# Kernel tuning notes

Hardware: AMD Instinct MI355X
Metric: run time of the kernel (lower is better)

## Reference

```python
import jax, jax.numpy as jnp
import numpy as np

M = 768   # num edges
N = 768   # num loops (== M because original tiles image_x with len(edge_x) for both)
C = 256
IMG = 1024
CAT = 3 * C + IMG  # 1792, 'sharing' suffix without '1d'/'noimage'
EPS = 1e-4


def _lin_block(x, W, b):
    # LinearBlock: Linear + ReLU
    return jax.nn.relu(x @ W + b)


def _pred_head(x, W1, b1, W2, b2):
    # Sequential(LinearBlock(256,64), Linear(64,1)) -> sigmoid -> flatten
    return jax.nn.sigmoid(_lin_block(x, W1, b1) @ W2 + b2).reshape(-1)


def setup_inputs() -> dict:
    key = jax.random.key(0)
    ks = jax.random.split(key, 24)
    s = 0.02
    return {
        "edge_x": jax.random.normal(ks[0], (M, C), jnp.float32),
        "loop_x": jax.random.normal(ks[1], (N, C), jnp.float32),
        "image_x": jax.random.normal(ks[2], (1, IMG), jnp.float32),
        "loop_edge_masks": (jax.random.uniform(ks[3], (N, M)) < 0.3).astype(jnp.float32),
        "edge_conflict_mask": (jax.random.uniform(ks[4], (M, M)) < 0.1).astype(jnp.float32),
        "loop_conflict_mask": (jax.random.uniform(ks[5], (N, N)) < 0.1).astype(jnp.float32),
        "loop_masks": jax.random.uniform(ks[6], (N, 64), jnp.float32),      # pass-through only
        "loop_edge_indices": jax.random.randint(ks[7], (N,), 0, M, jnp.int32),  # unused ('1d' off)
        "edge_info": jax.random.normal(ks[8], (M, 4), jnp.float32),         # unused ('1d' off)
        "W_e3": jax.random.normal(ks[9], (CAT, C), jnp.float32) * s,
        "b_e3": jnp.zeros((C,), jnp.float32),
        "W_l3": jax.random.normal(ks[10], (CAT, C), jnp.float32) * s,
        "b_l3": jnp.zeros((C,), jnp.float32),
        "W_ep1": jax.random.normal(ks[11], (C, 64), jnp.float32) * s,
        "b_ep1": jnp.zeros((64,), jnp.float32),
        "W_ep2": jax.random.normal(ks[12], (64, 1), jnp.float32) * s,
        "b_ep2": jnp.zeros((1,), jnp.float32),
        "W_lp1": jax.random.normal(ks[13], (C, 64), jnp.float32) * s,
        "b_lp1": jnp.zeros((64,), jnp.float32),
        "W_lp2": jax.random.normal(ks[14], (64, 1), jnp.float32) * s,
        "b_lp2": jnp.zeros((1,), jnp.float32),
    }


def reference(edge_x, loop_x, image_x, loop_edge_masks, edge_conflict_mask,
              loop_conflict_mask, loop_masks, loop_edge_indices, edge_info,
              W_e3, b_e3, W_l3, b_l3, W_ep1, b_ep1, W_ep2, b_ep2,
              W_lp1, b_lp1, W_lp2, b_lp2):
    # iteration-0 predictions (appended to results in original)
    e0 = _pred_head(edge_x, W_ep1, b_ep1, W_ep2, b_ep2)  # [M]
    l0 = _pred_head(loop_x, W_lp1, b_lp1, W_lp2, b_lp2)  # [N]

    # weights[n, m] = mask * |loop_pred[n] - edge_pred[m]|
    w = loop_edge_masks * jnp.abs(l0[:, None] - e0[None, :])  # [N, M]

    # weighted broadcast sums (einsum == unsqueeze-multiply-sum in the original)
    edge_x_from_loop = jnp.einsum('nm,nc->mc', w, loop_x) \
        / jnp.maximum(w.sum(0), EPS)[:, None]               # [M, C]
    loop_x_from_edge = jnp.einsum('nm,mc->nc', w, edge_x) \
        / jnp.maximum(w.sum(1), EPS)[:, None]               # [N, C]

    # conflict-masked max pooling (materializes [M,M,C]/[N,N,C] like the original)
    edge_x_from_conflict = jnp.max(edge_conflict_mask[:, :, None] * edge_x[None, :, :], axis=1)
    loop_x_from_conflict = jnp.max(loop_conflict_mask[:, :, None] * loop_x[None, :, :], axis=1)

    img_e = jnp.broadcast_to(image_x, (edge_x.shape[0], image_x.shape[1]))
    img_l = jnp.broadcast_to(image_x, (loop_x.shape[0], image_x.shape[1]))

    edge_x2 = _lin_block(jnp.concatenate([edge_x, edge_x_from_loop, edge_x_from_conflict, img_e], axis=-1), W_e3, b_e3)
    loop_x2 = _lin_block(jnp.concatenate([loop_x, loop_x_from_edge, loop_x_from_conflict, img_l], axis=-1), W_l3, b_l3)

    e1 = _pred_head(edge_x2, W_ep1, b_ep1, W_ep2, b_ep2)
    l1 = _pred_head(loop_x2, W_lp1, b_lp1, W_lp2, b_lp2)

    # original returns results=[[e0,l0,masks,loop_masks],[e1,l1,masks,loop_masks]];
    # masks are constant pass-throughs, so we return the predictions concatenated.
    return jnp.concatenate([e0, l0, e1, l1])  # [2*(M+N)] = [3072]
```

## Files before the change

kernel.cpp:

```cpp
#include <hip/hip_runtime.h>
#include <hip/hip_bf16.h>
#include <math.h>

#define MM 768
#define CC 256
#define EPSV 1e-4f

__device__ __forceinline__ float sigmoidf_(float x) { return 1.0f / (1.0f + expf(-x)); }

__global__ __launch_bounds__(256) void k_prep(
    const float* __restrict__ edge_x, const float* __restrict__ loop_x,
    const float* __restrict__ image_x,
    const float* __restrict__ ecm, const float* __restrict__ lcm,
    const float* __restrict__ We3, const float* __restrict__ Wl3,
    const float* __restrict__ Wep1, const float* __restrict__ bep1,
    const float* __restrict__ Wep2, const float* __restrict__ bep2,
    const float* __restrict__ Wlp1, const float* __restrict__ blp1,
    const float* __restrict__ Wlp2, const float* __restrict__ blp2,
    float* __restrict__ out, float* __restrict__ efc, float* __restrict__ lfc,
    float* __restrict__ imgpart)
{
    int bid = blockIdx.x;
    int t   = threadIdx.x;

    if (bid < 1536) {
        __shared__ int   s_cnt;
        __shared__ int   s_idx[MM];
        __shared__ float s_val[MM];
        bool isLoop = bid >= MM;
        int  m      = bid & (MM - 1);
        const float* mask = isLoop ? lcm : ecm;
        const float* x    = isLoop ? loop_x : edge_x;
        float*       o    = isLoop ? lfc : efc;

        if (t == 0) s_cnt = 0;
        __syncthreads();
        int lane = t & 63;
        #pragma unroll
        for (int r = 0; r < 3; ++r) {
            int j = t + r * 256;
            float v = mask[m * MM + j];
            bool nz = (v != 0.0f);
            unsigned long long b = __ballot(nz);
            int prefix = __popcll(b & ((1ull << lane) - 1ull));
            int cntw   = __popcll(b);
            int base = 0;
            if (lane == 0 && cntw) base = atomicAdd(&s_cnt, cntw);
            base = __shfl(base, 0, 64);
            if (nz) { s_idx[base + prefix] = j; s_val[base + prefix] = v; }
        }
        __syncthreads();
        int cnt = s_cnt;
        float init = (cnt < MM) ? 0.0f : -INFINITY;
        float a0 = init, a1 = init, a2 = init, a3 = init;
        int i = 0;
        for (; i + 4 <= cnt; i += 4) {
            a0 = fmaxf(a0, s_val[i + 0] * x[s_idx[i + 0] * CC + t]);
            a1 = fmaxf(a1, s_val[i + 1] * x[s_idx[i + 1] * CC + t]);
            a2 = fmaxf(a2, s_val[i + 2] * x[s_idx[i + 2] * CC + t]);
            a3 = fmaxf(a3, s_val[i + 3] * x[s_idx[i + 3] * CC + t]);
        }
        for (; i < cnt; ++i)
            a0 = fmaxf(a0, s_val[i] * x[s_idx[i] * CC + t]);
        o[m * CC + t] = fmaxf(fmaxf(a0, a1), fmaxf(a2, a3));

    } else if (bid < 1920) {
        int wave = t >> 6, lane = t & 63;
        int row  = (bid - 1536) * 4 + wave;
        const float *x, *W1, *b1, *W2;
        float b2v;
        if (row < MM) { x = edge_x + row * CC;        W1 = Wep1; b1 = bep1; W2 = Wep2; b2v = bep2[0]; }
        else          { x = loop_x + (row - MM) * CC; W1 = Wlp1; b1 = blp1; W2 = Wlp2; b2v = blp2[0]; }

        float a0 = 0.f, a1 = 0.f, a2 = 0.f, a3 = 0.f;
        for (int cc = 0; cc < CC; cc += 4) {
            float4 xv = *reinterpret_cast<const float4*>(x + cc);
            a0 = fmaf(xv.x, W1[(cc + 0) * 64 + lane], a0);
            a1 = fmaf(xv.y, W1[(cc + 1) * 64 + lane], a1);
            a2 = fmaf(xv.z, W1[(cc + 2) * 64 + lane], a2);
            a3 = fmaf(xv.w, W1[(cc + 3) * 64 + lane], a3);
        }
        float h = fmaxf(b1[lane] + ((a0 + a1) + (a2 + a3)), 0.0f);
        float p = h * W2[lane];
        #pragma unroll
        for (int off = 32; off; off >>= 1) p += __shfl_xor(p, off, 64);
        if (lane == 0) out[row] = sigmoidf_(p + b2v);

    } else {
        int sub   = bid - 1920;
        int chunk = sub & 3;
        int head  = sub >> 2;
        const float* W = head ? Wl3 : We3;
        int k0 = chunk * 256;
        float s = 0.0f;
        #pragma unroll 4
        for (int k = 0; k < 256; ++k)
            s = fmaf(image_x[k0 + k], W[(768 + k0 + k) * CC + t], s);
        imgpart[head * 1024 + chunk * 256 + t] = s;
    }
}

__global__ __launch_bounds__(512) void k_bsum(
    const float* __restrict__ lem, const float* __restrict__ edge_x,
    const float* __restrict__ loop_x, const float* __restrict__ pred,
    float* __restrict__ efl_p0, float* __restrict__ efl_p1,
    float* __restrict__ lfe_p0, float* __restrict__ lfe_p1)
{
    __shared__ float4 s_wv4[MM];
    __shared__ float  s_pw[8 * 4];
    __shared__ float  s_sum[4];
    __shared__ float  s_red[4 * 16 * 64];
    float* s_wv = reinterpret_cast<float*>(s_wv4);

    int bid  = blockIdx.x;
    int t    = threadIdx.x;
    int pair = bid >> 1, sh = bid & 1;
    const float* e0 = pred;
    const float* l0 = pred + MM;

    bool isE = pair < 192;
    int  r0  = (isE ? pair : pair - 192) * 4;
    const float* ownp = isE ? e0 : l0;
    const float* othp = isE ? l0 : e0;

    float own0 = ownp[r0], own1 = ownp[r0 + 1], own2 = ownp[r0 + 2], own3 = ownp[r0 + 3];

    int i_ = t & 3;
    float myown = own0;
    if (i_ == 1) myown = own1; else if (i_ == 2) myown = own2; else if (i_ == 3) myown = own3;
    float psum = 0.f;
    #pragma unroll
    for (int k = 0; k < 6; ++k) {
        int idx = t + k * 512;
        int s = idx >> 2;
        float lm = isE ? lem[s * MM + r0 + i_] : lem[(r0 + i_) * MM + s];
        float wv = lm * fabsf(othp[s] - myown);
        s_wv[idx] = wv;
        psum += wv;
    }
    #pragma unroll
    for (int off = 4; off < 64; off <<= 1) psum += __shfl_xor(psum, off, 64);
    int wave = t >> 6, lane = t & 63;
    if (lane < 4) s_pw[wave * 4 + lane] = psum;
    __syncthreads();
    if (t < 4) {
        float s = 0.f;
        #pragma unroll
        for (int w = 0; w < 8; ++w) s += s_pw[w * 4 + t];
        s_sum[t] = fmaxf(s, EPSV);
    }

    const float* xsrc = isE ? loop_x : edge_x;
    int s_base = sh * 384 + wave * 48;
    float acc[4][4];
    #pragma unroll
    for (int i = 0; i < 4; ++i)
        #pragma unroll
        for (int c = 0; c < 4; ++c) acc[i][c] = 0.f;

    #pragma unroll 4
    for (int j = 0; j < 48; ++j) {
        int s = s_base + j;
        float4 w4 = s_wv4[s];
        float4 xv = *reinterpret_cast<const float4*>(xsrc + s * CC + lane * 4);
        acc[0][0] = fmaf(w4.x, xv.x, acc[0][0]); acc[0][1] = fmaf(w4.x, xv.y, acc[0][1]);
        acc[0][2] = fmaf(w4.x, xv.z, acc[0][2]); acc[0][3] = fmaf(w4.x, xv.w, acc[0][3]);
        acc[1][0] = fmaf(w4.y, xv.x, acc[1][0]); acc[1][1] = fmaf(w4.y, xv.y, acc[1][1]);
        acc[1][2] = fmaf(w4.y, xv.z, acc[1][2]); acc[1][3] = fmaf(w4.y, xv.w, acc[1][3]);
        acc[2][0] = fmaf(w4.z, xv.x, acc[2][0]); acc[2][1] = fmaf(w4.z, xv.y, acc[2][1]);
        acc[2][2] = fmaf(w4.z, xv.z, acc[2][2]); acc[2][3] = fmaf(w4.z, xv.w, acc[2][3]);
        acc[3][0] = fmaf(w4.w, xv.x, acc[3][0]); acc[3][1] = fmaf(w4.w, xv.y, acc[3][1]);
        acc[3][2] = fmaf(w4.w, xv.z, acc[3][2]); acc[3][3] = fmaf(w4.w, xv.w, acc[3][3]);
    }

    if (wave >= 4) {
        #pragma unroll
        for (int i = 0; i < 4; ++i)
            #pragma unroll
            for (int c = 0; c < 4; ++c)
                s_red[(wave - 4) * 1024 + (i * 4 + c) * 64 + lane] = acc[i][c];
    }
    __syncthreads();
    if (wave < 4) {
        #pragma unroll
        for (int i = 0; i < 4; ++i)
            #pragma unroll
            for (int c = 0; c < 4; ++c)
                acc[i][c] += s_red[wave * 1024 + (i * 4 + c) * 64 + lane];
    }
    __syncthreads();
    if (wave == 2 || wave == 3) {
        #pragma unroll
        for (int i = 0; i < 4; ++i)
            #pragma unroll
            for (int c = 0; c < 4; ++c)
                s_red[(wave - 2) * 1024 + (i * 4 + c) * 64 + lane] = acc[i][c];
    }
    __syncthreads();
    if (wave < 2) {
        #pragma unroll
        for (int i = 0; i < 4; ++i)
            #pragma unroll
            for (int c = 0; c < 4; ++c)
                acc[i][c] += s_red[wave * 1024 + (i * 4 + c) * 64 + lane];
    }
    __syncthreads();
    if (wave == 1) {
        #pragma unroll
        for (int i = 0; i < 4; ++i)
            #pragma unroll
            for (int c = 0; c < 4; ++c)
                s_red[(i * 4 + c) * 64 + lane] = acc[i][c];
    }
    __syncthreads();
    if (wave == 0) {
        float* outp = isE ? (sh ? efl_p1 : efl_p0) : (sh ? lfe_p1 : lfe_p0);
        #pragma unroll
        for (int i = 0; i < 4; ++i) {
            float inv = 1.0f / s_sum[i];
            float4 o;
            o.x = (acc[i][0] + s_red[(i * 4 + 0) * 64 + lane]) * inv;
            o.y = (acc[i][1] + s_red[(i * 4 + 1) * 64 + lane]) * inv;
            o.z = (acc[i][2] + s_red[(i * 4 + 2) * 64 + lane]) * inv;
            o.w = (acc[i][3] + s_red[(i * 4 + 3) * 64 + lane]) * inv;
            *reinterpret_cast<float4*>(outp + (r0 + i) * CC + lane * 4) = o;
        }
    }
}

__global__ __launch_bounds__(512) void k_cat(
    const float* __restrict__ edge_x, const float* __restrict__ loop_x,
    const float* __restrict__ efl_p0, const float* __restrict__ efl_p1,
    const float* __restrict__ lfe_p0, const float* __restrict__ lfe_p1,
    const float* __restrict__ efc, const float* __restrict__ lfc,
    const float* __restrict__ We3, const float* __restrict__ be3,
    const float* __restrict__ Wl3, const float* __restrict__ bl3,
    const float* __restrict__ imgpart,
    const float* __restrict__ Wep1, const float* __restrict__ bep1,
    const float* __restrict__ Wep2, const float* __restrict__ bep2,
    const float* __restrict__ Wlp1, const float* __restrict__ blp1,
    const float* __restrict__ Wlp2, const float* __restrict__ blp2,
    float* __restrict__ out)
{
    __shared__ float s_red[4 * 16 * 64];
    __shared__ float s_act[4 * CC];
    __shared__ float s_h[8 * 64];

    int head = blockIdx.y;
    const float* W   = head ? Wl3 : We3;
    const float* b   = head ? bl3 : be3;
    const float* x0  = head ? loop_x : edge_x;
    const float* x1a = head ? lfe_p0 : efl_p0;
    const float* x1b = head ? lfe_p1 : efl_p1;
    const float* x2  = head ? lfc : efc;
    const float* ip  = imgpart + head * 1024;

    int m0 = blockIdx.x * 4;
    int t  = threadIdx.x;
    int wave = t >> 6, lane = t & 63;

    float acc[4][4];
    #pragma unroll
    for (int i = 0; i < 4; ++i)
        #pragma unroll
        for (int c = 0; c < 4; ++c) acc[i][c] = 0.f;

    int k0 = wave * 96;
    for (int jj = 0; jj < 96; jj += 4) {
        int k = k0 + jj;
        float4 xr[4];
        if (k < 256) {
            #pragma unroll
            for (int i = 0; i < 4; ++i)
                xr[i] = *reinterpret_cast<const float4*>(x0 + (m0 + i) * CC + k);
        } else if (k < 512) {
            int kk = k - 256;
            #pragma unroll
            for (int i = 0; i < 4; ++i) {
                float4 a = *reinterpret_cast<const float4*>(x1a + (m0 + i) * CC + kk);
                float4 bb = *reinterpret_cast<const float4*>(x1b + (m0 + i) * CC + kk);
                xr[i].x = a.x + bb.x; xr[i].y = a.y + bb.y;
                xr[i].z = a.z + bb.z; xr[i].w = a.w + bb.w;
            }
        } else {
            int kk = k - 512;
            #pragma unroll
            for (int i = 0; i < 4; ++i)
                xr[i] = *reinterpret_cast<const float4*>(x2 + (m0 + i) * CC + kk);
        }
        #pragma unroll
        for (int j = 0; j < 4; ++j) {
            float4 wv = *reinterpret_cast<const float4*>(W + (k + j) * CC + lane * 4);
            float xj0 = reinterpret_cast<const float*>(&xr[0])[j];
            float xj1 = reinterpret_cast<const float*>(&xr[1])[j];
            float xj2 = reinterpret_cast<const float*>(&xr[2])[j];
            float xj3 = reinterpret_cast<const float*>(&xr[3])[j];
            acc[0][0] = fmaf(xj0, wv.x, acc[0][0]); acc[0][1] = fmaf(xj0, wv.y, acc[0][1]);
            acc[0][2] = fmaf(xj0, wv.z, acc[0][2]); acc[0][3] = fmaf(xj0, wv.w, acc[0][3]);
            acc[1][0] = fmaf(xj1, wv.x, acc[1][0]); acc[1][1] = fmaf(xj1, wv.y, acc[1][1]);
            acc[1][2] = fmaf(xj1, wv.z, acc[1][2]); acc[1][3] = fmaf(xj1, wv.w, acc[1][3]);
            acc[2][0] = fmaf(xj2, wv.x, acc[2][0]); acc[2][1] = fmaf(xj2, wv.y, acc[2][1]);
            acc[2][2] = fmaf(xj2, wv.z, acc[2][2]); acc[2][3] = fmaf(xj2, wv.w, acc[2][3]);
            acc[3][0] = fmaf(xj3, wv.x, acc[3][0]); acc[3][1] = fmaf(xj3, wv.y, acc[3][1]);
            acc[3][2] = fmaf(xj3, wv.z, acc[3][2]); acc[3][3] = fmaf(xj3, wv.w, acc[3][3]);
        }
    }

    if (wave >= 4) {
        #pragma unroll
        for (int i = 0; i < 4; ++i)
            #pragma unroll
            for (int c = 0; c < 4; ++c)
                s_red[(wave - 4) * 1024 + (i * 4 + c) * 64 + lane] = acc[i][c];
    }
    __syncthreads();
    if (wave < 4) {
        #pragma unroll
        for (int i = 0; i < 4; ++i)
            #pragma unroll
            for (int c = 0; c < 4; ++c)
                acc[i][c] += s_red[wave * 1024 + (i * 4 + c) * 64 + lane];
    }
    __syncthreads();
    if (wave == 2 || wave == 3) {
        #pragma unroll
        for (int i = 0; i < 4; ++i)
            #pragma unroll
            for (int c = 0; c < 4; ++c)
                s_red[(wave - 2) * 1024 + (i * 4 + c) * 64 + lane] = acc[i][c];
    }
    __syncthreads();
    if (wave < 2) {
        #pragma unroll
        for (int i = 0; i < 4; ++i)
            #pragma unroll
            for (int c = 0; c < 4; ++c)
                acc[i][c] += s_red[wave * 1024 + (i * 4 + c) * 64 + lane];
    }
    __syncthreads();
    if (wave == 1) {
        #pragma unroll
        for (int i = 0; i < 4; ++i)
            #pragma unroll
            for (int c = 0; c < 4; ++c)
                s_red[(i * 4 + c) * 64 + lane] = acc[i][c];
    }
    __syncthreads();
    if (wave == 0) {
        float4 b4  = *reinterpret_cast<const float4*>(b + lane * 4);
        float4 i0  = *reinterpret_cast<const float4*>(ip + lane * 4);
        float4 i1  = *reinterpret_cast<const float4*>(ip + 256 + lane * 4);
        float4 i2  = *reinterpret_cast<const float4*>(ip + 512 + lane * 4);
        float4 i3  = *reinterpret_cast<const float4*>(ip + 768 + lane * 4);
        float bias[4] = { b4.x + i0.x + i1.x + i2.x + i3.x,
                          b4.y + i0.y + i1.y + i2.y + i3.y,
                          b4.z + i0.z + i1.z + i2.z + i3.z,
                          b4.w + i0.w + i1.w + i2.w + i3.w };
        #pragma unroll
        for (int i = 0; i < 4; ++i) {
            float4 o;
            o.x = fmaxf(acc[i][0] + s_red[(i * 4 + 0) * 64 + lane] + bias[0], 0.f);
            o.y = fmaxf(acc[i][1] + s_red[(i * 4 + 1) * 64 + lane] + bias[1], 0.f);
            o.z = fmaxf(acc[i][2] + s_red[(i * 4 + 2) * 64 + lane] + bias[2], 0.f);
            o.w = fmaxf(acc[i][3] + s_red[(i * 4 + 3) * 64 + lane] + bias[3], 0.f);
            *reinterpret_cast<float4*>(s_act + i * CC + lane * 4) = o;
        }
    }
    __syncthreads();

    int row = wave >> 1, khalf = wave & 1;
    const float* W1 = head ? Wlp1 : Wep1;
    const float* b1 = head ? blp1 : bep1;
    const float* W2 = head ? Wlp2 : Wep2;
    float b2v       = head ? blp2[0] : bep2[0];
    const float* xr = s_act + row * CC + khalf * 128;

    float a0 = 0.f, a1 = 0.f, a2 = 0.f, a3 = 0.f;
    for (int cc = 0; cc < 128; cc += 4) {
        float4 xv = *reinterpret_cast<const float4*>(xr + cc);
        int kb = khalf * 128 + cc;
        a0 = fmaf(xv.x, W1[(kb + 0) * 64 + lane], a0);
        a1 = fmaf(xv.y, W1[(kb + 1) * 64 + lane], a1);
        a2 = fmaf(xv.z, W1[(kb + 2) * 64 + lane], a2);
        a3 = fmaf(xv.w, W1[(kb + 3) * 64 + lane], a3);
    }
    s_h[wave * 64 + lane] = (a0 + a1) + (a2 + a3);
    __syncthreads();
    if (khalf == 0) {
        float hv = fmaxf(b1[lane] + s_h[wave * 64 + lane] + s_h[(wave + 1) * 64 + lane], 0.0f);
        float p = hv * W2[lane];
        #pragma unroll
        for (int off = 32; off; off >>= 1) p += __shfl_xor(p, off, 64);
        if (lane == 0) out[1536 + head * MM + m0 + row] = sigmoidf_(p + b2v);
    }
}

extern "C" void kernel_launch(void* const* d_in, const int* in_sizes, int n_in,
                              void* d_out, int out_size, void* d_ws, size_t ws_size,
                              hipStream_t stream)
{
    const float* edge_x  = (const float*)d_in[0];
    const float* loop_x  = (const float*)d_in[1];
    const float* image_x = (const float*)d_in[2];
    const float* lem     = (const float*)d_in[3];
    const float* ecm     = (const float*)d_in[4];
    const float* lcm     = (const float*)d_in[5];
    const float* We3  = (const float*)d_in[9];
    const float* be3  = (const float*)d_in[10];
    const float* Wl3  = (const float*)d_in[11];
    const float* bl3  = (const float*)d_in[12];
    const float* Wep1 = (const float*)d_in[13];
    const float* bep1 = (const float*)d_in[14];
    const float* Wep2 = (const float*)d_in[15];
    const float* bep2 = (const float*)d_in[16];
    const float* Wlp1 = (const float*)d_in[17];
    const float* blp1 = (const float*)d_in[18];
    const float* Wlp2 = (const float*)d_in[19];
    const float* blp2 = (const float*)d_in[20];

    float* out = (float*)d_out;
    float* ws  = (float*)d_ws;

    float* imgpart = ws;
    float* efl_p0  = ws + 2048;
    float* efl_p1  = efl_p0 + MM * CC;
    float* lfe_p0  = efl_p1 + MM * CC;
    float* lfe_p1  = lfe_p0 + MM * CC;
    float* efc     = lfe_p1 + MM * CC;
    float* lfc     = efc + MM * CC;

    k_prep<<<1928, 256, 0, stream>>>(edge_x, loop_x, image_x, ecm, lcm,
                                     We3, Wl3,
                                     Wep1, bep1, Wep2, bep2,
                                     Wlp1, blp1, Wlp2, blp2,
                                     out, efc, lfc, imgpart);

    k_bsum<<<768, 512, 0, stream>>>(lem, edge_x, loop_x, out,
                                    efl_p0, efl_p1, lfe_p0, lfe_p1);

    k_cat<<<dim3(192, 2), 512, 0, stream>>>(edge_x, loop_x,
                                            efl_p0, efl_p1, lfe_p0, lfe_p1,
                                            efc, lfc,
                                            We3, be3, Wl3, bl3, imgpart,
                                            Wep1, bep1, Wep2, bep2,
                                            Wlp1, blp1, Wlp2, blp2, out);
}
```

Baseline: 170.1 us.

## Move conflict max-pool into middle kernel and drop split-K partial buffers

The conflict-masked max pooling moves out of the first kernel into the second, which now has 384 weighted-sum blocks followed by 768 blocks that each handle two max-pool rows, sharing memory through a union. The weighted-sum blocks now cover all 768 source rows instead of splitting them across two blocks, so only one partial buffer per side is written and the concat GEMM no longer adds two partials. The goal is to shrink the first kernel so it finishes sooner, balance work across launches, and cut intermediate memory traffic. In exchange each weighted-sum block runs a loop twice as long, and there are half as many of them.

```diff
diff --git a/kernel.cpp b/kernel.cpp
--- a/kernel.cpp
+++ b/kernel.cpp
@@ -11,62 +11,19 @@
 __global__ __launch_bounds__(256) void k_prep(
     const float* __restrict__ edge_x, const float* __restrict__ loop_x,
     const float* __restrict__ image_x,
-    const float* __restrict__ ecm, const float* __restrict__ lcm,
     const float* __restrict__ We3, const float* __restrict__ Wl3,
     const float* __restrict__ Wep1, const float* __restrict__ bep1,
     const float* __restrict__ Wep2, const float* __restrict__ bep2,
     const float* __restrict__ Wlp1, const float* __restrict__ blp1,
     const float* __restrict__ Wlp2, const float* __restrict__ blp2,
-    float* __restrict__ out, float* __restrict__ efc, float* __restrict__ lfc,
-    float* __restrict__ imgpart)
+    float* __restrict__ out, float* __restrict__ imgpart)
 {
     int bid = blockIdx.x;
     int t   = threadIdx.x;
 
-    if (bid < 1536) {
-        __shared__ int   s_cnt;
-        __shared__ int   s_idx[MM];
-        __shared__ float s_val[MM];
-        bool isLoop = bid >= MM;
-        int  m      = bid & (MM - 1);
-        const float* mask = isLoop ? lcm : ecm;
-        const float* x    = isLoop ? loop_x : edge_x;
-        float*       o    = isLoop ? lfc : efc;
-
-        if (t == 0) s_cnt = 0;
-        __syncthreads();
-        int lane = t & 63;
-        #pragma unroll
-        for (int r = 0; r < 3; ++r) {
-            int j = t + r * 256;
-            float v = mask[m * MM + j];
-            bool nz = (v != 0.0f);
-            unsigned long long b = __ballot(nz);
-            int prefix = __popcll(b & ((1ull << lane) - 1ull));
-            int cntw   = __popcll(b);
-            int base = 0;
-            if (lane == 0 && cntw) base = atomicAdd(&s_cnt, cntw);
-            base = __shfl(base, 0, 64);
-            if (nz) { s_idx[base + prefix] = j; s_val[base + prefix] = v; }
-        }
-        __syncthreads();
-        int cnt = s_cnt;
-        float init = (cnt < MM) ? 0.0f : -INFINITY;
-        float a0 = init, a1 = init, a2 = init, a3 = init;
-        int i = 0;
-        for (; i + 4 <= cnt; i += 4) {
-            a0 = fmaxf(a0, s_val[i + 0] * x[s_idx[i + 0] * CC + t]);
-            a1 = fmaxf(a1, s_val[i + 1] * x[s_idx[i + 1] * CC + t]);
-            a2 = fmaxf(a2, s_val[i + 2] * x[s_idx[i + 2] * CC + t]);
-            a3 = fmaxf(a3, s_val[i + 3] * x[s_idx[i + 3] * CC + t]);
-        }
-        for (; i < cnt; ++i)
-            a0 = fmaxf(a0, s_val[i] * x[s_idx[i] * CC + t]);
-        o[m * CC + t] = fmaxf(fmaxf(a0, a1), fmaxf(a2, a3));
-
-    } else if (bid < 1920) {
+    if (bid < 384) {
         int wave = t >> 6, lane = t & 63;
-        int row  = (bid - 1536) * 4 + wave;
+        int row  = bid * 4 + wave;
         const float *x, *W1, *b1, *W2;
         float b2v;
         if (row < MM) { x = edge_x + row * CC;        W1 = Wep1; b1 = bep1; W2 = Wep2; b2v = bep2[0]; }
@@ -87,7 +44,7 @@
         if (lane == 0) out[row] = sigmoidf_(p + b2v);
 
     } else {
-        int sub   = bid - 1920;
+        int sub   = bid - 384;
         int chunk = sub & 3;
         int head  = sub >> 2;
         const float* W = head ? Wl3 : We3;
@@ -100,138 +57,181 @@
     }
 }
 
-__global__ __launch_bounds__(512) void k_bsum(
+__global__ __launch_bounds__(512) void k_mid(
     const float* __restrict__ lem, const float* __restrict__ edge_x,
     const float* __restrict__ loop_x, const float* __restrict__ pred,
-    float* __restrict__ efl_p0, float* __restrict__ efl_p1,
-    float* __restrict__ lfe_p0, float* __restrict__ lfe_p1)
+    const float* __restrict__ ecm, const float* __restrict__ lcm,
+    float* __restrict__ efl, float* __restrict__ lfe,
+    float* __restrict__ efc, float* __restrict__ lfc)
 {
-    __shared__ float4 s_wv4[MM];
-    __shared__ float  s_pw[8 * 4];
-    __shared__ float  s_sum[4];
-    __shared__ float  s_red[4 * 16 * 64];
-    float* s_wv = reinterpret_cast<float*>(s_wv4);
-
-    int bid  = blockIdx.x;
-    int t    = threadIdx.x;
-    int pair = bid >> 1, sh = bid & 1;
-    const float* e0 = pred;
-    const float* l0 = pred + MM;
-
-    bool isE = pair < 192;
-    int  r0  = (isE ? pair : pair - 192) * 4;
-    const float* ownp = isE ? e0 : l0;
-    const float* othp = isE ? l0 : e0;
-
-    float own0 = ownp[r0], own1 = ownp[r0 + 1], own2 = ownp[r0 + 2], own3 = ownp[r0 + 3];
-
-    int i_ = t & 3;
-    float myown = own0;
-    if (i_ == 1) myown = own1; else if (i_ == 2) myown = own2; else if (i_ == 3) myown = own3;
-    float psum = 0.f;
-    #pragma unroll
-    for (int k = 0; k < 6; ++k) {
-        int idx = t + k * 512;
-        int s = idx >> 2;
-        float lm = isE ? lem[s * MM + r0 + i_] : lem[(r0 + i_) * MM + s];
-        float wv = lm * fabsf(othp[s] - myown);
-        s_wv[idx] = wv;
-        psum += wv;
-    }
-    #pragma unroll
-    for (int off = 4; off < 64; off <<= 1) psum += __shfl_xor(psum, off, 64);
+    __shared__ union U {
+        struct { float4 wv4[MM]; float pw[32]; float sum[4]; float red[4096]; } b;
+        struct { int cnt[2]; int idx[2][MM]; float val[2][MM]; } c;
+    } u;
+
+    int bid = blockIdx.x;
+    int t   = threadIdx.x;
     int wave = t >> 6, lane = t & 63;
-    if (lane < 4) s_pw[wave * 4 + lane] = psum;
-    __syncthreads();
-    if (t < 4) {
-        float s = 0.f;
-        #pragma unroll
-        for (int w = 0; w < 8; ++w) s += s_pw[w * 4 + t];
-        s_sum[t] = fmaxf(s, EPSV);
-    }
-
-    const float* xsrc = isE ? loop_x : edge_x;
-    int s_base = sh * 384 + wave * 48;
-    float acc[4][4];
-    #pragma unroll
-    for (int i = 0; i < 4; ++i)
-        #pragma unroll
-        for (int c = 0; c < 4; ++c) acc[i][c] = 0.f;
-
-    #pragma unroll 4
-    for (int j = 0; j < 48; ++j) {
-        int s = s_base + j;
-        float4 w4 = s_wv4[s];
-        float4 xv = *reinterpret_cast<const float4*>(xsrc + s * CC + lane * 4);
-        acc[0][0] = fmaf(w4.x, xv.x, acc[0][0]); acc[0][1] = fmaf(w4.x, xv.y, acc[0][1]);
-        acc[0][2] = fmaf(w4.x, xv.z, acc[0][2]); acc[0][3] = fmaf(w4.x, xv.w, acc[0][3]);
-        acc[1][0] = fmaf(w4.y, xv.x, acc[1][0]); acc[1][1] = fmaf(w4.y, xv.y, acc[1][1]);
-        acc[1][2] = fmaf(w4.y, xv.z, acc[1][2]); acc[1][3] = fmaf(w4.y, xv.w, acc[1][3]);
-        acc[2][0] = fmaf(w4.z, xv.x, acc[2][0]); acc[2][1] = fmaf(w4.z, xv.y, acc[2][1]);
-        acc[2][2] = fmaf(w4.z, xv.z, acc[2][2]); acc[2][3] = fmaf(w4.z, xv.w, acc[2][3]);
-        acc[3][0] = fmaf(w4.w, xv.x, acc[3][0]); acc[3][1] = fmaf(w4.w, xv.y, acc[3][1]);
-        acc[3][2] = fmaf(w4.w, xv.z, acc[3][2]); acc[3][3] = fmaf(w4.w, xv.w, acc[3][3]);
-    }
-
-    if (wave >= 4) {
-        #pragma unroll
-        for (int i = 0; i < 4; ++i)
-            #pragma unroll
-            for (int c = 0; c < 4; ++c)
-                s_red[(wave - 4) * 1024 + (i * 4 + c) * 64 + lane] = acc[i][c];
-    }
-    __syncthreads();
-    if (wave < 4) {
-        #pragma unroll
-        for (int i = 0; i < 4; ++i)
-            #pragma unroll
-            for (int c = 0; c < 4; ++c)
-                acc[i][c] += s_red[wave * 1024 + (i * 4 + c) * 64 + lane];
-    }
-    __syncthreads();
-    if (wave == 2 || wave == 3) {
-        #pragma unroll
-        for (int i = 0; i < 4; ++i)
-            #pragma unroll
-            for (int c = 0; c < 4; ++c)
-                s_red[(wave - 2) * 1024 + (i * 4 + c) * 64 + lane] = acc[i][c];
-    }
-    __syncthreads();
-    if (wave < 2) {
-        #pragma unroll
-        for (int i = 0; i < 4; ++i)
-            #pragma unroll
-            for (int c = 0; c < 4; ++c)
-                acc[i][c] += s_red[wave * 1024 + (i * 4 + c) * 64 + lane];
-    }
-    __syncthreads();
-    if (wave == 1) {
-        #pragma unroll
-        for (int i = 0; i < 4; ++i)
-            #pragma unroll
-            for (int c = 0; c < 4; ++c)
-                s_red[(i * 4 + c) * 64 + lane] = acc[i][c];
-    }
-    __syncthreads();
-    if (wave == 0) {
-        float* outp = isE ? (sh ? efl_p1 : efl_p0) : (sh ? lfe_p1 : lfe_p0);
-        #pragma unroll
-        for (int i = 0; i < 4; ++i) {
-            float inv = 1.0f / s_sum[i];
-            float4 o;
-            o.x = (acc[i][0] + s_red[(i * 4 + 0) * 64 + lane]) * inv;
-            o.y = (acc[i][1] + s_red[(i * 4 + 1) * 64 + lane]) * inv;
-            o.z = (acc[i][2] + s_red[(i * 4 + 2) * 64 + lane]) * inv;
-            o.w = (acc[i][3] + s_red[(i * 4 + 3) * 64 + lane]) * inv;
-            *reinterpret_cast<float4*>(outp + (r0 + i) * CC + lane * 4) = o;
-        }
+
+    if (bid < 384) {
+        float* s_wv = reinterpret_cast<float*>(u.b.wv4);
+        const float* e0 = pred;
+        const float* l0 = pred + MM;
+
+        int  pair = bid;
+        bool isE  = pair < 192;
+        int  r0   = (isE ? pair : pair - 192) * 4;
+        const float* ownp = isE ? e0 : l0;
+        const float* othp = isE ? l0 : e0;
+
+        float own0 = ownp[r0], own1 = ownp[r0 + 1], own2 = ownp[r0 + 2], own3 = ownp[r0 + 3];
+
+        int i_ = t & 3;
+        float myown = own0;
+        if (i_ == 1) myown = own1; else if (i_ == 2) myown = own2; else if (i_ == 3) myown = own3;
+        float psum = 0.f;
+        #pragma unroll
+        for (int k = 0; k < 6; ++k) {
+            int idx = t + k * 512;
+            int s = idx >> 2;
+            float lm = isE ? lem[s * MM + r0 + i_] : lem[(r0 + i_) * MM + s];
+            float wv = lm * fabsf(othp[s] - myown);
+            s_wv[idx] = wv;
+            psum += wv;
+        }
+        #pragma unroll
+        for (int off = 4; off < 64; off <<= 1) psum += __shfl_xor(psum, off, 64);
+        if (lane < 4) u.b.pw[wave * 4 + lane] = psum;
+        __syncthreads();
+        if (t < 4) {
+            float s = 0.f;
+            #pragma unroll
+            for (int w = 0; w < 8; ++w) s += u.b.pw[w * 4 + t];
+            u.b.sum[t] = fmaxf(s, EPSV);
+        }
+
+        const float* xsrc = isE ? loop_x : edge_x;
+        int s_base = wave * 96;
+        float acc[4][4];
+        #pragma unroll
+        for (int i = 0; i < 4; ++i)
+            #pragma unroll
+            for (int c = 0; c < 4; ++c) acc[i][c] = 0.f;
+
+        #pragma unroll 4
+        for (int j = 0; j < 96; ++j) {
+            int s = s_base + j;
+            float4 w4 = u.b.wv4[s];
+            float4 xv = *reinterpret_cast<const float4*>(xsrc + s * CC + lane * 4);
+            acc[0][0] = fmaf(w4.x, xv.x, acc[0][0]); acc[0][1] = fmaf(w4.x, xv.y, acc[0][1]);
+            acc[0][2] = fmaf(w4.x, xv.z, acc[0][2]); acc[0][3] = fmaf(w4.x, xv.w, acc[0][3]);
+            acc[1][0] = fmaf(w4.y, xv.x, acc[1][0]); acc[1][1] = fmaf(w4.y, xv.y, acc[1][1]);
+            acc[1][2] = fmaf(w4.y, xv.z, acc[1][2]); acc[1][3] = fmaf(w4.y, xv.w, acc[1][3]);
+            acc[2][0] = fmaf(w4.z, xv.x, acc[2][0]); acc[2][1] = fmaf(w4.z, xv.y, acc[2][1]);
+            acc[2][2] = fmaf(w4.z, xv.z, acc[2][2]); acc[2][3] = fmaf(w4.z, xv.w, acc[2][3]);
+            acc[3][0] = fmaf(w4.w, xv.x, acc[3][0]); acc[3][1] = fmaf(w4.w, xv.y, acc[3][1]);
+            acc[3][2] = fmaf(w4.w, xv.z, acc[3][2]); acc[3][3] = fmaf(w4.w, xv.w, acc[3][3]);
+        }
+
+        if (wave >= 4) {
+            #pragma unroll
+            for (int i = 0; i < 4; ++i)
+                #pragma unroll
+                for (int c = 0; c < 4; ++c)
+                    u.b.red[(wave - 4) * 1024 + (i * 4 + c) * 64 + lane] = acc[i][c];
+        }
+        __syncthreads();
+        if (wave < 4) {
+            #pragma unroll
+            for (int i = 0; i < 4; ++i)
+                #pragma unroll
+                for (int c = 0; c < 4; ++c)
+                    acc[i][c] += u.b.red[wave * 1024 + (i * 4 + c) * 64 + lane];
+        }
+        __syncthreads();
+        if (wave == 2 || wave == 3) {
+            #pragma unroll
+            for (int i = 0; i < 4; ++i)
+                #pragma unroll
+                for (int c = 0; c < 4; ++c)
+                    u.b.red[(wave - 2) * 1024 + (i * 4 + c) * 64 + lane] = acc[i][c];
+        }
+        __syncthreads();
+        if (wave < 2) {
+            #pragma unroll
+            for (int i = 0; i < 4; ++i)
+                #pragma unroll
+                for (int c = 0; c < 4; ++c)
+                    acc[i][c] += u.b.red[wave * 1024 + (i * 4 + c) * 64 + lane];
+        }
+        __syncthreads();
+        if (wave == 1) {
+            #pragma unroll
+            for (int i = 0; i < 4; ++i)
+                #pragma unroll
+                for (int c = 0; c < 4; ++c)
+                    u.b.red[(i * 4 + c) * 64 + lane] = acc[i][c];
+        }
+        __syncthreads();
+        if (wave == 0) {
+            float* outp = isE ? efl : lfe;
+            #pragma unroll
+            for (int i = 0; i < 4; ++i) {
+                float inv = 1.0f / u.b.sum[i];
+                float4 o;
+                o.x = (acc[i][0] + u.b.red[(i * 4 + 0) * 64 + lane]) * inv;
+                o.y = (acc[i][1] + u.b.red[(i * 4 + 1) * 64 + lane]) * inv;
+                o.z = (acc[i][2] + u.b.red[(i * 4 + 2) * 64 + lane]) * inv;
+                o.w = (acc[i][3] + u.b.red[(i * 4 + 3) * 64 + lane]) * inv;
+                *reinterpret_cast<float4*>(outp + (r0 + i) * CC + lane * 4) = o;
+            }
+        }
+
+    } else {
+        int half = t >> 8;
+        int tt   = t & 255;
+        int rowg = (bid - 384) * 2 + half;
+        bool isLoop = rowg >= MM;
+        int  m      = rowg & (MM - 1);
+        const float* mask = isLoop ? lcm : ecm;
+        const float* x    = isLoop ? loop_x : edge_x;
+        float*       o    = isLoop ? lfc : efc;
+
+        if (tt == 0) u.c.cnt[half] = 0;
+        __syncthreads();
+        #pragma unroll
+        for (int r = 0; r < 3; ++r) {
+            int j = tt + r * 256;
+            float v = mask[m * MM + j];
+            bool nz = (v != 0.0f);
+            unsigned long long b = __ballot(nz);
+            int prefix = __popcll(b & ((1ull << lane) - 1ull));
+            int cntw   = __popcll(b);
+            int base = 0;
+            if (lane == 0 && cntw) base = atomicAdd(&u.c.cnt[half], cntw);
+            base = __shfl(base, 0, 64);
+            if (nz) { u.c.idx[half][base + prefix] = j; u.c.val[half][base + prefix] = v; }
+        }
+        __syncthreads();
+        int cnt = u.c.cnt[half];
+        float init = (cnt < MM) ? 0.0f : -INFINITY;
+        float a0 = init, a1 = init, a2 = init, a3 = init;
+        int i = 0;
+        for (; i + 4 <= cnt; i += 4) {
+            a0 = fmaxf(a0, u.c.val[half][i + 0] * x[u.c.idx[half][i + 0] * CC + tt]);
+            a1 = fmaxf(a1, u.c.val[half][i + 1] * x[u.c.idx[half][i + 1] * CC + tt]);
+            a2 = fmaxf(a2, u.c.val[half][i + 2] * x[u.c.idx[half][i + 2] * CC + tt]);
+            a3 = fmaxf(a3, u.c.val[half][i + 3] * x[u.c.idx[half][i + 3] * CC + tt]);
+        }
+        for (; i < cnt; ++i)
+            a0 = fmaxf(a0, u.c.val[half][i] * x[u.c.idx[half][i] * CC + tt]);
+        o[m * CC + tt] = fmaxf(fmaxf(a0, a1), fmaxf(a2, a3));
     }
 }
 
 __global__ __launch_bounds__(512) void k_cat(
     const float* __restrict__ edge_x, const float* __restrict__ loop_x,
-    const float* __restrict__ efl_p0, const float* __restrict__ efl_p1,
-    const float* __restrict__ lfe_p0, const float* __restrict__ lfe_p1,
+    const float* __restrict__ efl, const float* __restrict__ lfe,
     const float* __restrict__ efc, const float* __restrict__ lfc,
     const float* __restrict__ We3, const float* __restrict__ be3,
     const float* __restrict__ Wl3, const float* __restrict__ bl3,
@@ -247,13 +247,12 @@
     __shared__ float s_h[8 * 64];
 
     int head = blockIdx.y;
-    const float* W   = head ? Wl3 : We3;
-    const float* b   = head ? bl3 : be3;
-    const float* x0  = head ? loop_x : edge_x;
-    const float* x1a = head ? lfe_p0 : efl_p0;
-    const float* x1b = head ? lfe_p1 : efl_p1;
-    const float* x2  = head ? lfc : efc;
-    const float* ip  = imgpart + head * 1024;
+    const float* W  = head ? Wl3 : We3;
+    const float* b  = head ? bl3 : be3;
+    const float* x0 = head ? loop_x : edge_x;
+    const float* x1 = head ? lfe : efl;
+    const float* x2 = head ? lfc : efc;
+    const float* ip = imgpart + head * 1024;
 
     int m0 = blockIdx.x * 4;
     int t  = threadIdx.x;
@@ -276,12 +275,8 @@
         } else if (k < 512) {
             int kk = k - 256;
             #pragma unroll
-            for (int i = 0; i < 4; ++i) {
-                float4 a = *reinterpret_cast<const float4*>(x1a + (m0 + i) * CC + kk);
-                float4 bb = *reinterpret_cast<const float4*>(x1b + (m0 + i) * CC + kk);
-                xr[i].x = a.x + bb.x; xr[i].y = a.y + bb.y;
-                xr[i].z = a.z + bb.z; xr[i].w = a.w + bb.w;
-            }
+            for (int i = 0; i < 4; ++i)
+                xr[i] = *reinterpret_cast<const float4*>(x1 + (m0 + i) * CC + kk);
         } else {
             int kk = k - 512;
             #pragma unroll
@@ -422,25 +417,21 @@
     float* ws  = (float*)d_ws;
 
     float* imgpart = ws;
-    float* efl_p0  = ws + 2048;
-    float* efl_p1  = efl_p0 + MM * CC;
-    float* lfe_p0  = efl_p1 + MM * CC;
-    float* lfe_p1  = lfe_p0 + MM * CC;
-    float* efc     = lfe_p1 + MM * CC;
+    float* efl     = ws + 2048;
+    float* lfe     = efl + MM * CC;
+    float* efc     = lfe + MM * CC;
     float* lfc     = efc + MM * CC;
 
-    k_prep<<<1928, 256, 0, stream>>>(edge_x, loop_x, image_x, ecm, lcm,
-                                     We3, Wl3,
-                                     Wep1, bep1, Wep2, bep2,
-                                     Wlp1, blp1, Wlp2, blp2,
-                                     out, efc, lfc, imgpart);
-
-    k_bsum<<<768, 512, 0, stream>>>(lem, edge_x, loop_x, out,
-                                    efl_p0, efl_p1, lfe_p0, lfe_p1);
-
-    k_cat<<<dim3(192, 2), 512, 0, stream>>>(edge_x, loop_x,
-                                            efl_p0, efl_p1, lfe_p0, lfe_p1,
-                                            efc, lfc,
+    k_prep<<<392, 256, 0, stream>>>(edge_x, loop_x, image_x,
+                                    We3, Wl3,
+                                    Wep1, bep1, Wep2, bep2,
+                                    Wlp1, blp1, Wlp2, blp2,
+                                    out, imgpart);
+
+    k_mid<<<1152, 512, 0, stream>>>(lem, edge_x, loop_x, out, ecm, lcm,
+                                    efl, lfe, efc, lfc);
+
+    k_cat<<<dim3(192, 2), 512, 0, stream>>>(edge_x, loop_x, efl, lfe, efc, lfc,
                                             We3, be3, Wl3, bl3, imgpart,
                                             Wep1, bep1, Wep2, bep2,
                                             Wlp1, blp1, Wlp2, blp2, out);
```

After: 182.1 us. 1.07x slower.
